# Kernel tuning notes

Hardware: AMD Instinct MI355X
Metric: run time of the kernel (lower is better)

The kernel has to match this reference:

```python
import jax, jax.numpy as jnp
import numpy as np

# ---- constants derived from init_kwargs (level_i=0) ----
STRIDE = 8
BASE = 4 * STRIDE  # cfg['model.retina.anchor.base'] * stride = 32
SCALES = [1.0, 1.2599, 1.5874]
RATIOS = [[1.0, 1.0], [1.4, 0.7], [0.7, 1.4]]
ANCHOR_WH = jnp.asarray([[BASE * s * r[0], BASE * s * r[1]] for s in SCALES for r in RATIOS],
                        dtype=jnp.float32)  # [nA, 2]
POS_THRES = 0.5
NEG_THRES = 0.4
NCLS = 80


def _anchor_boxes(nA, nH, nW):
    """Anchor boxes in cxcywh, shape [nA, nH, nW, 4] (cx varies over W, cy over H, wh over A)."""
    a_cx = (jnp.arange(nW, dtype=jnp.float32) + 0.5) * STRIDE  # [nW]
    a_cy = (jnp.arange(nH, dtype=jnp.float32) + 0.5) * STRIDE  # [nH]
    cx = jnp.broadcast_to(a_cx[None, None, :, None], (nA, nH, nW, 1))
    cy = jnp.broadcast_to(a_cy[None, :, None, None], (nA, nH, nW, 1))
    wh = jnp.broadcast_to(ANCHOR_WH[:, None, None, :], (nA, nH, nW, 2))
    return jnp.concatenate([cx, cy, wh], axis=-1)


def _iou_cxcywh(anch, gt):
    """anch: [N,4] cxcywh, gt: [B,G,4] cxcywh -> iou [B,N,G]."""
    a_tl = anch[:, :2] - anch[:, 2:] * 0.5  # [N,2]
    a_br = anch[:, :2] + anch[:, 2:] * 0.5
    g_tl = gt[..., :2] - gt[..., 2:] * 0.5  # [B,G,2]
    g_br = gt[..., :2] + gt[..., 2:] * 0.5
    tl = jnp.maximum(a_tl[None, :, None, :], g_tl[:, None, :, :])  # [B,N,G,2]
    br = jnp.minimum(a_br[None, :, None, :], g_br[:, None, :, :])
    inter = jnp.prod(jnp.clip(br - tl, 0.0, None), axis=-1)  # [B,N,G]
    area_a = anch[:, 2] * anch[:, 3]          # [N]
    area_g = gt[..., 2] * gt[..., 3]          # [B,G]
    union = area_a[None, :, None] + area_g[:, None, :] - inter
    return inter / union


def setup_inputs() -> dict:
    key = jax.random.key(0)
    k1, k2, k3, k4, k5 = jax.random.split(key, 5)
    B, nA, nH, nW, nGT = 8, 9, 64, 64, 32
    t_xywh = jax.random.normal(k1, (B, nA, nH, nW, 4), dtype=jnp.float32) * 0.1
    cls_logits = jax.random.normal(k2, (B, nA, nH, nW, NCLS), dtype=jnp.float32)
    # GT boxes (cx, cy, w, h), valid inside a 512x512 image
    cxy = jax.random.uniform(k3, (B, nGT, 2), minval=32.0, maxval=480.0, dtype=jnp.float32)
    wh = jax.random.uniform(k4, (B, nGT, 2), minval=16.0, maxval=160.0, dtype=jnp.float32)
    gt_bboxes = jnp.concatenate([cxy, wh], axis=-1)
    gt_cats = jax.random.randint(k5, (B, nGT), 0, NCLS)
    return {"t_xywh": t_xywh, "cls_logits": cls_logits, "gt_bboxes": gt_bboxes,
            "gt_cats": gt_cats, "img_h": 512, "img_w": 512}


def reference(t_xywh, cls_logits, gt_bboxes, gt_cats, img_h, img_w):
    B, nA, nH, nW, _ = t_xywh.shape
    nCls = cls_logits.shape[-1]
    N = nA * nH * nW

    anch = _anchor_boxes(nA, nH, nW).reshape(N, 4)  # [N,4]

    ious = _iou_cxcywh(anch, gt_bboxes)             # [B,N,G]
    iou_with_gt = jnp.max(ious, axis=-1)            # [B,N]
    gt_idx = jnp.argmax(ious, axis=-1)              # [B,N]

    pos = iou_with_gt > POS_THRES                   # [B,N]
    neg = iou_with_gt < NEG_THRES
    penalty = pos | neg

    # gather matched GT box / category per anchor
    gb = jnp.take_along_axis(gt_bboxes, gt_idx[:, :, None], axis=1)  # [B,N,4]
    gc = jnp.take_along_axis(gt_cats, gt_idx, axis=1)                # [B,N]

    tgt_xy = (gb[..., :2] - anch[None, :, :2]) / anch[None, :, 2:]
    tgt_wh = jnp.log(gb[..., 2:] / anch[None, :, 2:] + 1e-8)
    tgt_xywh = jnp.concatenate([tgt_xy, tgt_wh], axis=-1)            # [B,N,4]

    t_flat = t_xywh.reshape(B, N, 4)
    posf = pos.astype(t_flat.dtype)
    loss_xywh = jnp.sum(posf[..., None] * (t_flat - tgt_xywh) ** 2)

    # class targets: one-hot at positive anchors, zeros elsewhere
    tgt_cls = jax.nn.one_hot(gc, nCls, dtype=t_flat.dtype) * posf[..., None]  # [B,N,C]
    x = cls_logits.reshape(B, N, nCls)
    # stable BCE-with-logits, summed per image over penalty anchors
    bce = jnp.maximum(x, 0.0) - x * tgt_cls + jnp.log1p(jnp.exp(-jnp.abs(x)))
    penf = penalty.astype(x.dtype)
    im_loss_cls = jnp.sum(penf[..., None] * bce, axis=(1, 2))   # [B]
    num_pos = jnp.sum(posf, axis=1)                             # [B]
    loss_cls = jnp.sum(im_loss_cls / (num_pos + 1.0))

    loss = (loss_xywh + loss_cls) / B
    return loss
```

## Files before the change

kernel.cpp:

```cpp
#include <hip/hip_runtime.h>

#define NCLS   80
#define NB     8
#define NGT    32
#define NANCH  36864
#define APB    128
#define NTHR   256
#define NBLK   2304
#define BLKS_PER_IMG 288
#define KI     10

#define LOG2E 1.4426950408889634f
#define LN2   0.6931471805599453f

__device__ __constant__ float c_aw[9] = {
    (float)(32.0 * 1.0    * 1.0), (float)(32.0 * 1.0    * 1.4), (float)(32.0 * 1.0    * 0.7),
    (float)(32.0 * 1.2599 * 1.0), (float)(32.0 * 1.2599 * 1.4), (float)(32.0 * 1.2599 * 0.7),
    (float)(32.0 * 1.5874 * 1.0), (float)(32.0 * 1.5874 * 1.4), (float)(32.0 * 1.5874 * 0.7)};
__device__ __constant__ float c_ah[9] = {
    (float)(32.0 * 1.0    * 1.0), (float)(32.0 * 1.0    * 0.7), (float)(32.0 * 1.0    * 1.4),
    (float)(32.0 * 1.2599 * 1.0), (float)(32.0 * 1.2599 * 0.7), (float)(32.0 * 1.2599 * 1.4),
    (float)(32.0 * 1.5874 * 1.0), (float)(32.0 * 1.5874 * 0.7), (float)(32.0 * 1.5874 * 1.4)};

#define COMP(X, K)                                                    \
    {                                                                 \
        const float m  = mk[K];                                       \
        const float t0 = __builtin_amdgcn_exp2f((X).x * LOG2E);       \
        const float t1 = __builtin_amdgcn_exp2f((X).y * LOG2E);       \
        const float t2 = __builtin_amdgcn_exp2f((X).z * LOG2E);       \
        const float t3 = __builtin_amdgcn_exp2f((X).w * LOG2E);       \
        const float P  = ((1.0f + t0) * (1.0f + t1)) *                \
                         ((1.0f + t2) * (1.0f + t3));                 \
        l2 += m * __builtin_amdgcn_logf(P);                           \
    }

__global__ __launch_bounds__(NTHR, 8) void retina_main(
    const float* __restrict__ t_xywh,
    const float* __restrict__ cls_logits,
    const float* __restrict__ gt_bboxes,
    const int*   __restrict__ gt_cats,
    float4* __restrict__ part)
{
    __shared__ float s_best[NTHR];
    __shared__ int   s_bi[NTHR];
    __shared__ float s_mask[APB];
    __shared__ float s_red[4 * 4];

    const int tid = threadIdx.x;
    const int blk = blockIdx.x;
    const int b   = blk / BLKS_PER_IMG;
    const int la0 = tid & (APB - 1);
    const int gh  = tid >> 7;

    const float4* base = (const float4*)cls_logits + (size_t)blk * (APB * NCLS / 4);

    float4 P0 = base[0 * NTHR + tid];
    float4 P1 = base[1 * NTHR + tid];
    float4 P2 = base[2 * NTHR + tid];
    float4 P3 = base[3 * NTHR + tid];

    const float4* gt4  = (const float4*)gt_bboxes + b * NGT;
    const int*    gcat = gt_cats + b * NGT;

    const int n  = (blk % BLKS_PER_IMG) * APB + la0;
    const int a  = n >> 12;
    const int hy = (n >> 6) & 63;
    const int wx = n & 63;
    const float acx = (wx + 0.5f) * 8.0f;
    const float acy = (hy + 0.5f) * 8.0f;
    const float aw  = c_aw[a];
    const float ah  = c_ah[a];

    float best = -1.0f;
    int   bi   = 0;
    {
#pragma clang fp contract(off)
        const float a_tlx = acx - aw * 0.5f, a_tly = acy - ah * 0.5f;
        const float a_brx = acx + aw * 0.5f, a_bry = acy + ah * 0.5f;
        const float area_a = aw * ah;
        const int g0 = gh * 16;
#pragma unroll
        for (int j = 0; j < 16; ++j) {
            const int gg = g0 + j;
            const float4 gb = gt4[gg];
            const float g_tlx = gb.x - gb.z * 0.5f, g_tly = gb.y - gb.w * 0.5f;
            const float g_brx = gb.x + gb.z * 0.5f, g_bry = gb.y + gb.w * 0.5f;
            float dx = fminf(a_brx, g_brx) - fmaxf(a_tlx, g_tlx);
            float dy = fminf(a_bry, g_bry) - fmaxf(a_tly, g_tly);
            dx = fmaxf(dx, 0.0f);
            dy = fmaxf(dy, 0.0f);
            const float inter = dx * dy;
            const float uni   = area_a + gb.z * gb.w - inter;
            const float iou   = inter * __builtin_amdgcn_rcpf(uni);
            if (iou > best) { best = iou; bi = gg; }
        }
    }
    s_best[tid] = best;
    s_bi[tid]   = bi;
    __syncthreads();

    float lx = 0.0f, pcnt = 0.0f, hot = 0.0f;
    if (tid < APB) {
        const float bhi = s_best[tid + APB];
        if (bhi > best) { best = bhi; bi = s_bi[tid + APB]; }
        const bool pos = best > 0.5f;
        const bool neg = best < 0.4f;
        if (pos) {
#pragma clang fp contract(off)
            const int cat = gcat[bi];
            pcnt = 1.0f;
            hot  = cls_logits[((size_t)blk * APB + tid) * NCLS + cat];
            const float4 g = gt4[bi];
            const float4 t = ((const float4*)t_xywh)[(size_t)b * NANCH + n];
            const float tx = (g.x - acx) / aw;
            const float ty = (g.y - acy) / ah;
            const float tw = logf(g.z / aw + 1e-8f);
            const float th = logf(g.w / ah + 1e-8f);
            const float d0 = t.x - tx, d1 = t.y - ty, d2 = t.z - tw, d3 = t.w - th;
            lx = d0 * d0 + d1 * d1 + d2 * d2 + d3 * d3;
        }
        s_mask[tid] = (pos | neg) ? 1.0f : 0.0f;
    }
    __syncthreads();

    float mk[KI];
#pragma unroll
    for (int k = 0; k < KI; ++k)
        mk[k] = s_mask[(k * NTHR + tid) / 20];

    float l2 = 0.0f;
    COMP(P0, 0)  P0 = base[4 * NTHR + tid];
    COMP(P1, 1)  P1 = base[5 * NTHR + tid];
    COMP(P2, 2)  P2 = base[6 * NTHR + tid];
    COMP(P3, 3)  P3 = base[7 * NTHR + tid];
    COMP(P0, 4)  P0 = base[8 * NTHR + tid];
    COMP(P1, 5)  P1 = base[9 * NTHR + tid];
    COMP(P2, 6)
    COMP(P3, 7)
    COMP(P0, 8)
    COMP(P1, 9)

    float v0 = l2, v1 = lx, v2 = pcnt, v3 = hot;
    for (int o = 32; o > 0; o >>= 1) {
        v0 += __shfl_down(v0, o);
        v1 += __shfl_down(v1, o);
        v2 += __shfl_down(v2, o);
        v3 += __shfl_down(v3, o);
    }
    const int wave = tid >> 6;
    if ((tid & 63) == 0) {
        s_red[wave * 4 + 0] = v0;
        s_red[wave * 4 + 1] = v1;
        s_red[wave * 4 + 2] = v2;
        s_red[wave * 4 + 3] = v3;
    }
    __syncthreads();
    if (tid == 0) {
        float q0 = 0.0f, q1 = 0.0f, q2 = 0.0f, q3 = 0.0f;
        for (int w2 = 0; w2 < 4; ++w2) {
            q0 += s_red[w2 * 4 + 0];
            q1 += s_red[w2 * 4 + 1];
            q2 += s_red[w2 * 4 + 2];
            q3 += s_red[w2 * 4 + 3];
        }
        part[blk] = make_float4(q0, q1, q2, q3);
    }
}

__global__ __launch_bounds__(256) void retina_final(
    const float4* __restrict__ part, float* __restrict__ out)
{
    __shared__ float s_l2[NB], s_pc[NB], s_ht[NB], s_lxr[NB];
    const int tid = threadIdx.x;
    const int img = tid >> 5, l = tid & 31;

    float l2s = 0.0f, lxs = 0.0f, pcs = 0.0f, hts = 0.0f;
    for (int i = l; i < BLKS_PER_IMG; i += 32) {
        const float4 p = part[img * BLKS_PER_IMG + i];
        l2s += p.x; lxs += p.y; pcs += p.z; hts += p.w;
    }
    for (int o = 16; o > 0; o >>= 1) {
        l2s += __shfl_xor(l2s, o);
        lxs += __shfl_xor(lxs, o);
        pcs += __shfl_xor(pcs, o);
        hts += __shfl_xor(hts, o);
    }
    if (l == 0) { s_l2[img] = l2s; s_pc[img] = pcs; s_ht[img] = hts; s_lxr[img] = lxs; }
    __syncthreads();

    if (tid == 0) {
        float s = 0.0f, lxt = 0.0f;
        for (int bb = 0; bb < NB; ++bb) {
            lxt += s_lxr[bb];
            const float lc_b = LN2 * s_l2[bb] - s_ht[bb];
            s += lc_b / (s_pc[bb] + 1.0f);
        }
        out[0] = (lxt + s) / (float)NB;
    }
}

extern "C" void kernel_launch(void* const* d_in, const int* in_sizes, int n_in,
                              void* d_out, int out_size, void* d_ws, size_t ws_size,
                              hipStream_t stream)
{
    const float* t_xywh     = (const float*)d_in[0];
    const float* cls_logits = (const float*)d_in[1];
    const float* gt_bboxes  = (const float*)d_in[2];
    const int*   gt_cats    = (const int*)d_in[3];

    float4* part = (float4*)d_ws;

    retina_main<<<NBLK, NTHR, 0, stream>>>(t_xywh, cls_logits, gt_bboxes, gt_cats, part);
    retina_final<<<1, 256, 0, stream>>>(part, (float*)d_out);
}
```

Baseline: 26.23 us.

## Fuse final reduction into main kernel via atomics and last-block finish

Removes the separate final reduction kernel. Each block atomically adds its partial sums into per-image accumulators and bumps a completion counter, and the last block to finish computes the final loss. A hipMemsetAsync zeroes the accumulators before launch. This trades a kernel launch for atomic contention on a few addresses plus a memset node, and it makes the float summation order nondeterministic.

```diff
diff --git a/kernel.cpp b/kernel.cpp
--- a/kernel.cpp
+++ b/kernel.cpp
@@ -12,6 +12,8 @@
 
 #define LOG2E 1.4426950408889634f
 #define LN2   0.6931471805599453f
+
+#define ACC_N 25
 
 __device__ __constant__ float c_aw[9] = {
     (float)(32.0 * 1.0    * 1.0), (float)(32.0 * 1.0    * 1.4), (float)(32.0 * 1.0    * 0.7),
@@ -39,12 +41,16 @@
     const float* __restrict__ cls_logits,
     const float* __restrict__ gt_bboxes,
     const int*   __restrict__ gt_cats,
-    float4* __restrict__ part)
+    float* __restrict__ acc,
+    unsigned int* __restrict__ cnt,
+    float* __restrict__ out)
 {
     __shared__ float s_best[NTHR];
     __shared__ int   s_bi[NTHR];
     __shared__ float s_mask[APB];
     __shared__ float s_red[4 * 4];
+    __shared__ float s_acc[ACC_N];
+    __shared__ int   s_last;
 
     const int tid = threadIdx.x;
     const int blk = blockIdx.x;
@@ -155,6 +161,7 @@
         s_red[wave * 4 + 3] = v3;
     }
     __syncthreads();
+
     if (tid == 0) {
         float q0 = 0.0f, q1 = 0.0f, q2 = 0.0f, q3 = 0.0f;
         for (int w2 = 0; w2 < 4; ++w2) {
@@ -163,39 +170,29 @@
             q2 += s_red[w2 * 4 + 2];
             q3 += s_red[w2 * 4 + 3];
         }
-        part[blk] = make_float4(q0, q1, q2, q3);
-    }
-}
-
-__global__ __launch_bounds__(256) void retina_final(
-    const float4* __restrict__ part, float* __restrict__ out)
-{
-    __shared__ float s_l2[NB], s_pc[NB], s_ht[NB], s_lxr[NB];
-    const int tid = threadIdx.x;
-    const int img = tid >> 5, l = tid & 31;
-
-    float l2s = 0.0f, lxs = 0.0f, pcs = 0.0f, hts = 0.0f;
-    for (int i = l; i < BLKS_PER_IMG; i += 32) {
-        const float4 p = part[img * BLKS_PER_IMG + i];
-        l2s += p.x; lxs += p.y; pcs += p.z; hts += p.w;
-    }
-    for (int o = 16; o > 0; o >>= 1) {
-        l2s += __shfl_xor(l2s, o);
-        lxs += __shfl_xor(lxs, o);
-        pcs += __shfl_xor(pcs, o);
-        hts += __shfl_xor(hts, o);
-    }
-    if (l == 0) { s_l2[img] = l2s; s_pc[img] = pcs; s_ht[img] = hts; s_lxr[img] = lxs; }
-    __syncthreads();
-
-    if (tid == 0) {
-        float s = 0.0f, lxt = 0.0f;
-        for (int bb = 0; bb < NB; ++bb) {
-            lxt += s_lxr[bb];
-            const float lc_b = LN2 * s_l2[bb] - s_ht[bb];
-            s += lc_b / (s_pc[bb] + 1.0f);
-        }
-        out[0] = (lxt + s) / (float)NB;
+        atomicAdd(&acc[1 + b], q0);
+        if (q1 != 0.0f) atomicAdd(&acc[0], q1);
+        if (q2 != 0.0f) atomicAdd(&acc[9 + b], q2);
+        if (q3 != 0.0f) atomicAdd(&acc[17 + b], q3);
+        asm volatile("s_waitcnt vmcnt(0)" ::: "memory");
+        const unsigned old = atomicAdd(cnt, 1u);
+        s_last = (old == NBLK - 1u) ? 1 : 0;
+    }
+    __syncthreads();
+
+    if (s_last) {
+        if (tid < ACC_N)
+            s_acc[tid] = __hip_atomic_load(&acc[tid], __ATOMIC_RELAXED,
+                                           __HIP_MEMORY_SCOPE_AGENT);
+        __syncthreads();
+        if (tid == 0) {
+            float s = 0.0f;
+            for (int bb = 0; bb < NB; ++bb) {
+                const float lc_b = LN2 * s_acc[1 + bb] - s_acc[17 + bb];
+                s += lc_b / (s_acc[9 + bb] + 1.0f);
+            }
+            out[0] = (s_acc[0] + s) / (float)NB;
+        }
     }
 }
 
@@ -208,8 +205,10 @@
     const float* gt_bboxes  = (const float*)d_in[2];
     const int*   gt_cats    = (const int*)d_in[3];
 
-    float4* part = (float4*)d_ws;
-
-    retina_main<<<NBLK, NTHR, 0, stream>>>(t_xywh, cls_logits, gt_bboxes, gt_cats, part);
-    retina_final<<<1, 256, 0, stream>>>(part, (float*)d_out);
+    float*        acc = (float*)d_ws;
+    unsigned int* cnt = (unsigned int*)d_ws + ACC_N;
+
+    hipMemsetAsync(d_ws, 0, (ACC_N + 1) * sizeof(float), stream);
+    retina_main<<<NBLK, NTHR, 0, stream>>>(t_xywh, cls_logits, gt_bboxes, gt_cats,
+                                           acc, cnt, (float*)d_out);
 }
```

Result: slower. 58.00 us (+121.1%).
